# Optimization experiments

Measured on AMD Instinct MI355X. Metric: run time of the kernel, lower is better.

The kernel has to match this reference:

```python
import jax, jax.numpy as jnp
import numpy as np

B, L, R, DV = 4, 4096, 8, 64

def setup_inputs() -> dict:
    key = jax.random.key(0)
    k1, k2, k3, k4 = jax.random.split(key, 4)
    return {
        "v": jax.random.normal(k1, (B, L, DV), dtype=jnp.float32),
        "mask": jax.random.randint(k2, (B, 1, L), 0, 2, dtype=jnp.int32),
        "random_attn_1": jax.random.normal(k3, (B, L, R), dtype=jnp.float32),
        "random_attn_2": jax.random.normal(k4, (B, R, L), dtype=jnp.float32),
        "len_q": L,
    }

def reference(v, mask, random_attn_1, random_attn_2, len_q):
    # rank-8 low-rank synthesis of attention scores: [B, len_q, len_q]
    Bm = mask.shape[0]
    scores = jnp.einsum("blr,brm->blm",
                        random_attn_1[:Bm, :len_q, :],
                        random_attn_2[:Bm, :, :len_q])
    scores = jnp.where(mask == 0, jnp.float32(-1e9), scores)
    attn = jax.nn.softmax(scores, axis=-1)  # dropout omitted (eval mode)
    out = jnp.einsum("blm,bmd->bld", attn, v[:Bm, :len_q, :])
    return out, attn
```

## Files before the change

kernel.cpp:

```cpp
#include <hip/hip_runtime.h>
#include <hip/hip_bf16.h>

#define BB  4
#define LL  4096
#define RR  8
#define DVV 64

typedef __bf16 bf16x8 __attribute__((ext_vector_type(8)));
typedef __bf16 bf16x4 __attribute__((ext_vector_type(4)));
typedef float  f32x4  __attribute__((ext_vector_type(4)));
typedef int    i32x4  __attribute__((ext_vector_type(4)));

#define LGKM_BARRIER() \
  asm volatile("s_waitcnt lgkmcnt(0)\n\ts_barrier" ::: "memory")

__global__ __launch_bounds__(256) void prep_kernel(
    const float* __restrict__ v, __bf16* __restrict__ vF) {
  __shared__ __bf16 tl[64][72];
  const int blk = blockIdx.x;
  const int b   = blk >> 6;
  const int m0  = (blk & 63) << 6;
  const int tid = threadIdx.x;

  const float* vb = v + (((size_t)(b * LL + m0)) << 6);
#pragma unroll
  for (int i = 0; i < 16; ++i) {
    const int idx = (i << 8) + tid;
    tl[idx & 63][idx >> 6] = (__bf16)vb[idx];
  }
  __syncthreads();

  const int wv = tid >> 6, ln = tid & 63;
#pragma unroll
  for (int i = 0; i < 2; ++i) {
    const int u  = wv + (i << 2);
    const int cb = u >> 2, gg = u & 3;
    const int d  = gg * 16 + (ln & 15);
    const int c  = cb * 32 + ((ln >> 4) << 3);
    const size_t unit = ((size_t)(b * 128 + (m0 >> 5) + cb) << 2) + gg;
    *(bf16x8*)(vF + (unit << 9) + (ln << 3)) = *(const bf16x8*)&tl[d][c];
  }
}

__global__ __launch_bounds__(512, 4) void attn_main(
    const float* __restrict__ ra1, const float* __restrict__ ra2,
    const int* __restrict__ mask, const __bf16* __restrict__ vF,
    float* __restrict__ out, float* __restrict__ attn) {
  __shared__ __bf16 pbuf[8 * 8 * 512];
  __shared__ float  red[8][8];

  const int wg   = blockIdx.x;
  const int b    = wg >> 9;
  const int row0 = (wg & 511) << 3;
  const int tid  = threadIdx.x;
  const int wave = tid >> 6;
  const int lane = tid & 63;
  const int W    = wave << 9;

  const float* r2 = ra2 + (size_t)b * (RR * LL) + W + (lane << 2);
  f32x4 rA[RR], rB[RR];
#pragma unroll
  for (int r = 0; r < RR; ++r) {
    rA[r] = *(const f32x4*)(r2 + r * LL);
    rB[r] = *(const f32x4*)(r2 + r * LL + 256);
  }
  const int* mp = mask + (size_t)b * LL + W + (lane << 2);
  const i32x4 mAv = *(const i32x4*)mp;
  const i32x4 mBv = *(const i32x4*)(mp + 256);
  f32x4 mA, mB;
#pragma unroll
  for (int j = 0; j < 4; ++j) {
    mA[j] = mAv[j] ? 1.0f : 0.0f;
    mB[j] = mBv[j] ? 1.0f : 0.0f;
  }

  const float* a_base = ra1 + ((size_t)b * LL + row0) * RR;
  char* const  pw     = (char*)pbuf + (wave << 13);

  float part[8];
#pragma unroll
  for (int i = 0; i < 8; ++i) {
    const float* ap = a_base + i * RR;
    f32x4 sA = {0.f, 0.f, 0.f, 0.f}, sB = {0.f, 0.f, 0.f, 0.f};
#pragma unroll
    for (int r = 0; r < RR; ++r) {
      const float a = ap[r];
#pragma unroll
      for (int j = 0; j < 4; ++j) {
        sA[j] = fmaf(a, rA[r][j], sA[j]);
        sB[j] = fmaf(a, rB[r][j], sB[j]);
      }
    }
    f32x4 eA, eB;
#pragma unroll
    for (int j = 0; j < 4; ++j) {
      eA[j] = __expf(sA[j]) * mA[j];
      eB[j] = __expf(sB[j]) * mB[j];
    }
    part[i] = ((eA[0] + eA[1]) + (eA[2] + eA[3])) +
              ((eB[0] + eB[1]) + (eB[2] + eB[3]));

    bf16x4 pA, pB;
#pragma unroll
    for (int j = 0; j < 4; ++j) { pA[j] = (__bf16)eA[j]; pB[j] = (__bf16)eB[j]; }
    const int swz = (i & 7) << 4;
    *(bf16x4*)(pw + (i << 10) + (((lane << 3)) ^ swz))       = pA;
    *(bf16x4*)(pw + (i << 10) + ((512 + (lane << 3)) ^ swz)) = pB;
  }
#pragma unroll
  for (int s = 1; s < 64; s <<= 1)
#pragma unroll
    for (int i = 0; i < 8; ++i) part[i] += __shfl_xor(part[i], s);
  if (lane == 0) {
#pragma unroll
    for (int i = 0; i < 8; ++i) red[i][wave] = part[i];
  }
  LGKM_BARRIER();

  float rs = 0.f;
#pragma unroll
  for (int v = 0; v < 8; ++v) rs += red[wave][v];
  const float rinv_w = 1.0f / rs;

  const int lrow = lane & 15, kg = lane >> 4;
  const int lr8  = lrow & 7;
  f32x4 acc[4];
#pragma unroll
  for (int g = 0; g < 4; ++g) acc[g] = (f32x4){0.f, 0.f, 0.f, 0.f};
  const __bf16* vFb = vF + ((size_t)b << 18);
  float* arow = attn + ((size_t)b * LL + row0 + wave) * LL;

#pragma unroll
  for (int t = 0; t < 16; ++t) {
    const bf16x8 af = *(const bf16x8*)(
        pw + (lr8 << 10) + (((t << 6) + (kg << 4)) ^ (lr8 << 4)));
    const __bf16* vblk =
        vFb + ((size_t)((wave << 4) + t) << 11) + (lane << 3);
#pragma unroll
    for (int g = 0; g < 4; ++g) {
      const bf16x8 bf = *(const bf16x8*)(vblk + (g << 9));
      acc[g] =
          __builtin_amdgcn_mfma_f32_16x16x32_bf16(af, bf, acc[g], 0, 0, 0);
    }
    const bf16x4 q = *(const bf16x4*)(
        (const char*)pbuf + ((t >> 1) << 13) + (wave << 10) + ((t & 1) << 9) +
        ((lane << 3) ^ ((wave & 7) << 4)));
    f32x4 o;
#pragma unroll
    for (int j = 0; j < 4; ++j) o[j] = (float)q[j] * rinv_w;
    *(f32x4*)(arow + (t << 8) + (lane << 2)) = o;
  }

  LGKM_BARRIER();
  float* osum = (float*)pbuf;
  if (kg < 2) {
#pragma unroll
    for (int g = 0; g < 4; ++g)
#pragma unroll
      for (int ii = 0; ii < 4; ++ii)
        osum[(wave * 8 + kg * 4 + ii) * 64 + g * 16 + lrow] = acc[g][ii];
  }
  LGKM_BARRIER();

  if (tid < 128) {
    const int orow = tid >> 4;
    const int d    = (tid & 15) << 2;
    f32x4 o = {0.f, 0.f, 0.f, 0.f};
#pragma unroll
    for (int w = 0; w < 8; ++w) {
      const f32x4 rr = *(const f32x4*)(osum + ((w * 8 + orow) << 6) + d);
#pragma unroll
      for (int j = 0; j < 4; ++j) o[j] += rr[j];
    }
    float rt = 0.f;
#pragma unroll
    for (int w = 0; w < 8; ++w) rt += red[orow][w];
    const float rinv_o = 1.0f / rt;
#pragma unroll
    for (int j = 0; j < 4; ++j) o[j] *= rinv_o;
    *(f32x4*)(out + ((size_t)b * LL + row0 + orow) * DVV + d) = o;
  }
}

extern "C" void kernel_launch(void* const* d_in, const int* in_sizes, int n_in,
                              void* d_out, int out_size, void* d_ws,
                              size_t ws_size, hipStream_t stream) {
  (void)in_sizes; (void)n_in; (void)out_size; (void)ws_size;
  const float* v    = (const float*)d_in[0];
  const int*   mask = (const int*)d_in[1];
  const float* ra1  = (const float*)d_in[2];
  const float* ra2  = (const float*)d_in[3];

  float* out  = (float*)d_out;
  float* attn = out + (size_t)BB * LL * DVV;

  __bf16* vF = (__bf16*)d_ws;

  hipLaunchKernelGGL(prep_kernel, dim3(BB * (LL / 64)), dim3(256), 0, stream,
                     v, vF);
  hipLaunchKernelGGL(attn_main, dim3(BB * LL / 8), dim3(512), 0, stream,
                     ra1, ra2, mask, vF, out, attn);
}
```

Before: 316.8 us.

## Specialize waves: add store waves for attn output, loop four row blocks per workgroup

The main kernel now launches 512 workgroups of 10 waves, each looping over four 8-row blocks. Eight compute waves do the scores, exp and MFMA while two extra waves handle writing the normalized attention rows. The 8-wave partial output reduction is split into a two-stage reduction through a smaller shared buffer. The intent is to overlap the large attn store traffic with compute and to spread the ra2 register loads across two halves, which lowers register pressure. The cost is more barriers per iteration and fewer workgroups in flight.

```diff
diff --git a/kernel.cpp b/kernel.cpp
--- a/kernel.cpp
+++ b/kernel.cpp
@@ -42,143 +42,183 @@
   }
 }
 
-__global__ __launch_bounds__(512, 4) void attn_main(
+__global__ __launch_bounds__(640, 5) void attn_main(
     const float* __restrict__ ra1, const float* __restrict__ ra2,
     const int* __restrict__ mask, const __bf16* __restrict__ vF,
     float* __restrict__ out, float* __restrict__ attn) {
   __shared__ __bf16 pbuf[8 * 8 * 512];
+  __shared__ float  osum4[4 * 8 * 64];
   __shared__ float  red[8][8];
 
   const int wg   = blockIdx.x;
-  const int b    = wg >> 9;
-  const int row0 = (wg & 511) << 3;
+  const int b    = wg >> 7;
+  const int blk0 = (wg & 127) << 2;
   const int tid  = threadIdx.x;
   const int wave = tid >> 6;
   const int lane = tid & 63;
-  const int W    = wave << 9;
-
-  const float* r2 = ra2 + (size_t)b * (RR * LL) + W + (lane << 2);
-  f32x4 rA[RR], rB[RR];
-#pragma unroll
-  for (int r = 0; r < RR; ++r) {
-    rA[r] = *(const f32x4*)(r2 + r * LL);
-    rB[r] = *(const f32x4*)(r2 + r * LL + 256);
-  }
-  const int* mp = mask + (size_t)b * LL + W + (lane << 2);
-  const i32x4 mAv = *(const i32x4*)mp;
-  const i32x4 mBv = *(const i32x4*)(mp + 256);
-  f32x4 mA, mB;
-#pragma unroll
-  for (int j = 0; j < 4; ++j) {
-    mA[j] = mAv[j] ? 1.0f : 0.0f;
-    mB[j] = mBv[j] ? 1.0f : 0.0f;
-  }
-
-  const float* a_base = ra1 + ((size_t)b * LL + row0) * RR;
-  char* const  pw     = (char*)pbuf + (wave << 13);
-
-  float part[8];
-#pragma unroll
-  for (int i = 0; i < 8; ++i) {
-    const float* ap = a_base + i * RR;
-    f32x4 sA = {0.f, 0.f, 0.f, 0.f}, sB = {0.f, 0.f, 0.f, 0.f};
-#pragma unroll
-    for (int r = 0; r < RR; ++r) {
-      const float a = ap[r];
-#pragma unroll
-      for (int j = 0; j < 4; ++j) {
-        sA[j] = fmaf(a, rA[r][j], sA[j]);
-        sB[j] = fmaf(a, rB[r][j], sB[j]);
-      }
-    }
-    f32x4 eA, eB;
-#pragma unroll
-    for (int j = 0; j < 4; ++j) {
-      eA[j] = __expf(sA[j]) * mA[j];
-      eB[j] = __expf(sB[j]) * mB[j];
-    }
-    part[i] = ((eA[0] + eA[1]) + (eA[2] + eA[3])) +
-              ((eB[0] + eB[1]) + (eB[2] + eB[3]));
-
-    bf16x4 pA, pB;
-#pragma unroll
-    for (int j = 0; j < 4; ++j) { pA[j] = (__bf16)eA[j]; pB[j] = (__bf16)eB[j]; }
-    const int swz = (i & 7) << 4;
-    *(bf16x4*)(pw + (i << 10) + (((lane << 3)) ^ swz))       = pA;
-    *(bf16x4*)(pw + (i << 10) + ((512 + (lane << 3)) ^ swz)) = pB;
-  }
-#pragma unroll
-  for (int s = 1; s < 64; s <<= 1)
-#pragma unroll
-    for (int i = 0; i < 8; ++i) part[i] += __shfl_xor(part[i], s);
-  if (lane == 0) {
-#pragma unroll
-    for (int i = 0; i < 8; ++i) red[i][wave] = part[i];
-  }
-  LGKM_BARRIER();
-
-  float rs = 0.f;
-#pragma unroll
-  for (int v = 0; v < 8; ++v) rs += red[wave][v];
-  const float rinv_w = 1.0f / rs;
-
+  const int cw   = wave & 7;
+  const int W    = cw << 9;
   const int lrow = lane & 15, kg = lane >> 4;
   const int lr8  = lrow & 7;
-  f32x4 acc[4];
-#pragma unroll
-  for (int g = 0; g < 4; ++g) acc[g] = (f32x4){0.f, 0.f, 0.f, 0.f};
+
+  const float* r2 = ra2 + (size_t)b * (RR * LL) + W + (lane << 2);
+  const int*   mp = mask + (size_t)b * LL + W + (lane << 2);
+
+  f32x4 mA = {0.f, 0.f, 0.f, 0.f}, mB = {0.f, 0.f, 0.f, 0.f};
+  if (wave < 8) {
+    const i32x4 mAv = *(const i32x4*)mp;
+    const i32x4 mBv = *(const i32x4*)(mp + 256);
+#pragma unroll
+    for (int j = 0; j < 4; ++j) {
+      mA[j] = mAv[j] ? 1.0f : 0.0f;
+      mB[j] = mBv[j] ? 1.0f : 0.0f;
+    }
+  }
   const __bf16* vFb = vF + ((size_t)b << 18);
-  float* arow = attn + ((size_t)b * LL + row0 + wave) * LL;
-
-#pragma unroll
-  for (int t = 0; t < 16; ++t) {
-    const bf16x8 af = *(const bf16x8*)(
-        pw + (lr8 << 10) + (((t << 6) + (kg << 4)) ^ (lr8 << 4)));
-    const __bf16* vblk =
-        vFb + ((size_t)((wave << 4) + t) << 11) + (lane << 3);
-#pragma unroll
-    for (int g = 0; g < 4; ++g) {
-      const bf16x8 bf = *(const bf16x8*)(vblk + (g << 9));
-      acc[g] =
-          __builtin_amdgcn_mfma_f32_16x16x32_bf16(af, bf, acc[g], 0, 0, 0);
-    }
-    const bf16x4 q = *(const bf16x4*)(
-        (const char*)pbuf + ((t >> 1) << 13) + (wave << 10) + ((t & 1) << 9) +
-        ((lane << 3) ^ ((wave & 7) << 4)));
-    f32x4 o;
-#pragma unroll
-    for (int j = 0; j < 4; ++j) o[j] = (float)q[j] * rinv_w;
-    *(f32x4*)(arow + (t << 8) + (lane << 2)) = o;
-  }
-
-  LGKM_BARRIER();
-  float* osum = (float*)pbuf;
-  if (kg < 2) {
-#pragma unroll
-    for (int g = 0; g < 4; ++g)
-#pragma unroll
-      for (int ii = 0; ii < 4; ++ii)
-        osum[(wave * 8 + kg * 4 + ii) * 64 + g * 16 + lrow] = acc[g][ii];
-  }
-  LGKM_BARRIER();
-
-  if (tid < 128) {
-    const int orow = tid >> 4;
-    const int d    = (tid & 15) << 2;
-    f32x4 o = {0.f, 0.f, 0.f, 0.f};
-#pragma unroll
-    for (int w = 0; w < 8; ++w) {
-      const f32x4 rr = *(const f32x4*)(osum + ((w * 8 + orow) << 6) + d);
-#pragma unroll
-      for (int j = 0; j < 4; ++j) o[j] += rr[j];
-    }
-    float rt = 0.f;
-#pragma unroll
-    for (int w = 0; w < 8; ++w) rt += red[orow][w];
-    const float rinv_o = 1.0f / rt;
-#pragma unroll
-    for (int j = 0; j < 4; ++j) o[j] *= rinv_o;
-    *(f32x4*)(out + ((size_t)b * LL + row0 + orow) * DVV + d) = o;
+  char* const   pw  = (char*)pbuf + (cw << 13);
+
+#pragma unroll 1
+  for (int jj = 0; jj < 4; ++jj) {
+    const int row0 = (blk0 + jj) << 3;
+
+    if (wave < 8) {
+      const float* a_base = ra1 + ((size_t)b * LL + row0) * RR;
+      float part[8];
+      {
+        f32x4 rr_[RR];
+#pragma unroll
+        for (int r = 0; r < RR; ++r) rr_[r] = *(const f32x4*)(r2 + r * LL);
+#pragma unroll
+        for (int i = 0; i < 8; ++i) {
+          const float* ap = a_base + i * RR;
+          f32x4 s = {0.f, 0.f, 0.f, 0.f};
+#pragma unroll
+          for (int r = 0; r < RR; ++r)
+#pragma unroll
+            for (int j = 0; j < 4; ++j) s[j] = fmaf(ap[r], rr_[r][j], s[j]);
+          f32x4 e;
+#pragma unroll
+          for (int j = 0; j < 4; ++j) e[j] = __expf(s[j]) * mA[j];
+          part[i] = (e[0] + e[1]) + (e[2] + e[3]);
+          bf16x4 p;
+#pragma unroll
+          for (int j = 0; j < 4; ++j) p[j] = (__bf16)e[j];
+          *(bf16x4*)(pw + (i << 10) + ((lane << 3) ^ (i << 4))) = p;
+        }
+      }
+      {
+        f32x4 rr_[RR];
+#pragma unroll
+        for (int r = 0; r < RR; ++r)
+          rr_[r] = *(const f32x4*)(r2 + r * LL + 256);
+#pragma unroll
+        for (int i = 0; i < 8; ++i) {
+          const float* ap = a_base + i * RR;
+          f32x4 s = {0.f, 0.f, 0.f, 0.f};
+#pragma unroll
+          for (int r = 0; r < RR; ++r)
+#pragma unroll
+            for (int j = 0; j < 4; ++j) s[j] = fmaf(ap[r], rr_[r][j], s[j]);
+          f32x4 e;
+#pragma unroll
+          for (int j = 0; j < 4; ++j) e[j] = __expf(s[j]) * mB[j];
+          part[i] += (e[0] + e[1]) + (e[2] + e[3]);
+          bf16x4 p;
+#pragma unroll
+          for (int j = 0; j < 4; ++j) p[j] = (__bf16)e[j];
+          *(bf16x4*)(pw + (i << 10) + (512 + ((lane << 3) ^ (i << 4)))) = p;
+        }
+      }
+#pragma unroll
+      for (int s = 1; s < 64; s <<= 1)
+#pragma unroll
+        for (int i = 0; i < 8; ++i) part[i] += __shfl_xor(part[i], s);
+      if (lane == 0) {
+#pragma unroll
+        for (int i = 0; i < 8; ++i) red[i][cw] = part[i];
+      }
+    }
+    LGKM_BARRIER();
+
+    f32x4 acc[4];
+    if (wave < 8) {
+#pragma unroll
+      for (int g = 0; g < 4; ++g) acc[g] = (f32x4){0.f, 0.f, 0.f, 0.f};
+#pragma unroll
+      for (int t = 0; t < 16; ++t) {
+        const bf16x8 af = *(const bf16x8*)(
+            pw + (lr8 << 10) + (((t << 6) + (kg << 4)) ^ (lr8 << 4)));
+        const __bf16* vblk =
+            vFb + ((size_t)((cw << 4) + t) << 11) + (lane << 3);
+#pragma unroll
+        for (int g = 0; g < 4; ++g) {
+          const bf16x8 bf = *(const bf16x8*)(vblk + (g << 9));
+          acc[g] =
+              __builtin_amdgcn_mfma_f32_16x16x32_bf16(af, bf, acc[g], 0, 0, 0);
+        }
+      }
+      if (wave >= 4 && kg < 2) {
+#pragma unroll
+        for (int g = 0; g < 4; ++g)
+#pragma unroll
+          for (int ii = 0; ii < 4; ++ii)
+            osum4[((wave - 4) * 8 + kg * 4 + ii) * 64 + g * 16 + lrow] =
+                acc[g][ii];
+      }
+      LGKM_BARRIER();
+      if (wave < 4 && kg < 2) {
+#pragma unroll
+        for (int g = 0; g < 4; ++g)
+#pragma unroll
+          for (int ii = 0; ii < 4; ++ii)
+            osum4[(wave * 8 + kg * 4 + ii) * 64 + g * 16 + lrow] +=
+                acc[g][ii];
+      }
+    } else {
+      const int w2 = (wave - 8) << 2;
+#pragma unroll
+      for (int rr2 = 0; rr2 < 4; ++rr2) {
+        const int r = w2 + rr2;
+        float rs = 0.f;
+#pragma unroll
+        for (int v2 = 0; v2 < 8; ++v2) rs += red[r][v2];
+        const float rinv_r = 1.0f / rs;
+        float* arow =
+            attn + ((size_t)b * LL + row0 + r) * LL + (lane << 2);
+#pragma unroll
+        for (int t = 0; t < 16; ++t) {
+          const bf16x4 q = *(const bf16x4*)(
+              (const char*)pbuf + ((t >> 1) << 13) + (r << 10) +
+              ((t & 1) << 9) + ((lane << 3) ^ (r << 4)));
+          f32x4 o;
+#pragma unroll
+          for (int j = 0; j < 4; ++j) o[j] = (float)q[j] * rinv_r;
+          *(f32x4*)(arow + (t << 8)) = o;
+        }
+      }
+      LGKM_BARRIER();
+    }
+    LGKM_BARRIER();
+
+    if (tid < 128) {
+      const int orow = tid >> 4;
+      const int d    = (tid & 15) << 2;
+      f32x4 o = {0.f, 0.f, 0.f, 0.f};
+#pragma unroll
+      for (int w = 0; w < 4; ++w) {
+        const f32x4 rr = *(const f32x4*)(osum4 + ((w * 8 + orow) << 6) + d);
+#pragma unroll
+        for (int j = 0; j < 4; ++j) o[j] += rr[j];
+      }
+      float rt = 0.f;
+#pragma unroll
+      for (int w = 0; w < 8; ++w) rt += red[orow][w];
+      const float rinv_o = 1.0f / rt;
+#pragma unroll
+      for (int j = 0; j < 4; ++j) o[j] *= rinv_o;
+      *(f32x4*)(out + ((size_t)b * LL + row0 + orow) * DVV + d) = o;
+    }
+    LGKM_BARRIER();
   }
 }
 
@@ -198,6 +238,6 @@
 
   hipLaunchKernelGGL(prep_kernel, dim3(BB * (LL / 64)), dim3(256), 0, stream,
                      v, vF);
-  hipLaunchKernelGGL(attn_main, dim3(BB * LL / 8), dim3(512), 0, stream,
+  hipLaunchKernelGGL(attn_main, dim3(512), dim3(640), 0, stream,
                      ra1, ra2, mask, vF, out, attn);
 }
```

After: 634.6 us. +100.3%, slower.

## Pipeline attn row stores with score computation in two-row stages

Applied to the files above, without the earlier changes.

Splits the eight-row score computation into four stages of two rows. Each stage gets its own cross-wave sum reduction and barrier, and the normalized attention rows from the previous stage are written out while the next stage computes. Each wave now writes its own column slice of every row instead of whole rows. This spreads the large attn store traffic across the score phase rather than putting it all after the MFMA loop. The cost is four barriers instead of one, plus different store coalescing.

```diff
diff --git a/kernel.cpp b/kernel.cpp
--- a/kernel.cpp
+++ b/kernel.cpp
@@ -76,51 +76,105 @@
 
   const float* a_base = ra1 + ((size_t)b * LL + row0) * RR;
   char* const  pw     = (char*)pbuf + (wave << 13);
-
-  float part[8];
-#pragma unroll
-  for (int i = 0; i < 8; ++i) {
-    const float* ap = a_base + i * RR;
-    f32x4 sA = {0.f, 0.f, 0.f, 0.f}, sB = {0.f, 0.f, 0.f, 0.f};
-#pragma unroll
-    for (int r = 0; r < RR; ++r) {
-      const float a = ap[r];
+  float* attn_base    = attn + ((size_t)b * LL + row0) * LL + W + (lane << 2);
+
+  float rv0 = 0.f, rv1 = 0.f;
+
+#pragma unroll
+  for (int st = 0; st < 4; ++st) {
+    if (st > 0) {
+#pragma unroll
+      for (int h = 0; h < 2; ++h) {
+        const int i   = 2 * (st - 1) + h;
+        const float rv = h ? rv1 : rv0;
+        const int swz = (i & 7) << 4;
+        const bf16x4 qA =
+            *(const bf16x4*)(pw + (i << 10) + ((lane << 3) ^ swz));
+        const bf16x4 qB =
+            *(const bf16x4*)(pw + (i << 10) + (512 + ((lane << 3) ^ swz)));
+        f32x4 oA, oB;
+#pragma unroll
+        for (int j = 0; j < 4; ++j) {
+          oA[j] = (float)qA[j] * rv;
+          oB[j] = (float)qB[j] * rv;
+        }
+        *(f32x4*)(attn_base + (size_t)i * LL)       = oA;
+        *(f32x4*)(attn_base + (size_t)i * LL + 256) = oB;
+      }
+      __builtin_amdgcn_sched_barrier(0);
+    }
+
+    float part[2];
+#pragma unroll
+    for (int h = 0; h < 2; ++h) {
+      const int i = 2 * st + h;
+      const float* ap = a_base + i * RR;
+      f32x4 sA = {0.f, 0.f, 0.f, 0.f}, sB = {0.f, 0.f, 0.f, 0.f};
+#pragma unroll
+      for (int r = 0; r < RR; ++r) {
+        const float a = ap[r];
+#pragma unroll
+        for (int j = 0; j < 4; ++j) {
+          sA[j] = fmaf(a, rA[r][j], sA[j]);
+          sB[j] = fmaf(a, rB[r][j], sB[j]);
+        }
+      }
+      f32x4 eA, eB;
 #pragma unroll
       for (int j = 0; j < 4; ++j) {
-        sA[j] = fmaf(a, rA[r][j], sA[j]);
-        sB[j] = fmaf(a, rB[r][j], sB[j]);
+        eA[j] = __expf(sA[j]) * mA[j];
+        eB[j] = __expf(sB[j]) * mB[j];
       }
-    }
-    f32x4 eA, eB;
+      part[h] = ((eA[0] + eA[1]) + (eA[2] + eA[3])) +
+                ((eB[0] + eB[1]) + (eB[2] + eB[3]));
+
+      bf16x4 pA, pB;
+#pragma unroll
+      for (int j = 0; j < 4; ++j) { pA[j] = (__bf16)eA[j]; pB[j] = (__bf16)eB[j]; }
+      const int swz = (i & 7) << 4;
+      *(bf16x4*)(pw + (i << 10) + ((lane << 3) ^ swz))         = pA;
+      *(bf16x4*)(pw + (i << 10) + (512 + ((lane << 3) ^ swz))) = pB;
+    }
+#pragma unroll
+    for (int s = 1; s < 64; s <<= 1) {
+      part[0] += __shfl_xor(part[0], s);
+      part[1] += __shfl_xor(part[1], s);
+    }
+    if (lane == 0) {
+      red[2 * st][wave]     = part[0];
+      red[2 * st + 1][wave] = part[1];
+    }
+    LGKM_BARRIER();
+    {
+      const f32x4 r00 = *(const f32x4*)&red[2 * st][0];
+      const f32x4 r01 = *(const f32x4*)&red[2 * st][4];
+      const f32x4 r10 = *(const f32x4*)&red[2 * st + 1][0];
+      const f32x4 r11 = *(const f32x4*)&red[2 * st + 1][4];
+      rv0 = 1.0f / (((r00[0] + r00[1]) + (r00[2] + r00[3])) +
+                    ((r01[0] + r01[1]) + (r01[2] + r01[3])));
+      rv1 = 1.0f / (((r10[0] + r10[1]) + (r10[2] + r10[3])) +
+                    ((r11[0] + r11[1]) + (r11[2] + r11[3])));
+    }
+  }
+
+#pragma unroll
+  for (int h = 0; h < 2; ++h) {
+    const int i    = 6 + h;
+    const float rv = h ? rv1 : rv0;
+    const int swz  = (i & 7) << 4;
+    const bf16x4 qA = *(const bf16x4*)(pw + (i << 10) + ((lane << 3) ^ swz));
+    const bf16x4 qB =
+        *(const bf16x4*)(pw + (i << 10) + (512 + ((lane << 3) ^ swz)));
+    f32x4 oA, oB;
 #pragma unroll
     for (int j = 0; j < 4; ++j) {
-      eA[j] = __expf(sA[j]) * mA[j];
-      eB[j] = __expf(sB[j]) * mB[j];
-    }
-    part[i] = ((eA[0] + eA[1]) + (eA[2] + eA[3])) +
-              ((eB[0] + eB[1]) + (eB[2] + eB[3]));
-
-    bf16x4 pA, pB;
-#pragma unroll
-    for (int j = 0; j < 4; ++j) { pA[j] = (__bf16)eA[j]; pB[j] = (__bf16)eB[j]; }
-    const int swz = (i & 7) << 4;
-    *(bf16x4*)(pw + (i << 10) + (((lane << 3)) ^ swz))       = pA;
-    *(bf16x4*)(pw + (i << 10) + ((512 + (lane << 3)) ^ swz)) = pB;
-  }
-#pragma unroll
-  for (int s = 1; s < 64; s <<= 1)
-#pragma unroll
-    for (int i = 0; i < 8; ++i) part[i] += __shfl_xor(part[i], s);
-  if (lane == 0) {
-#pragma unroll
-    for (int i = 0; i < 8; ++i) red[i][wave] = part[i];
-  }
-  LGKM_BARRIER();
-
-  float rs = 0.f;
-#pragma unroll
-  for (int v = 0; v < 8; ++v) rs += red[wave][v];
-  const float rinv_w = 1.0f / rs;
+      oA[j] = (float)qA[j] * rv;
+      oB[j] = (float)qB[j] * rv;
+    }
+    *(f32x4*)(attn_base + (size_t)i * LL)       = oA;
+    *(f32x4*)(attn_base + (size_t)i * LL + 256) = oB;
+  }
+  __builtin_amdgcn_sched_barrier(0);
 
   const int lrow = lane & 15, kg = lane >> 4;
   const int lr8  = lrow & 7;
@@ -128,8 +182,6 @@
 #pragma unroll
   for (int g = 0; g < 4; ++g) acc[g] = (f32x4){0.f, 0.f, 0.f, 0.f};
   const __bf16* vFb = vF + ((size_t)b << 18);
-  float* arow = attn + ((size_t)b * LL + row0 + wave) * LL;
-
 #pragma unroll
   for (int t = 0; t < 16; ++t) {
     const bf16x8 af = *(const bf16x8*)(
@@ -142,13 +194,6 @@
       acc[g] =
           __builtin_amdgcn_mfma_f32_16x16x32_bf16(af, bf, acc[g], 0, 0, 0);
     }
-    const bf16x4 q = *(const bf16x4*)(
-        (const char*)pbuf + ((t >> 1) << 13) + (wave << 10) + ((t & 1) << 9) +
-        ((lane << 3) ^ ((wave & 7) << 4)));
-    f32x4 o;
-#pragma unroll
-    for (int j = 0; j < 4; ++j) o[j] = (float)q[j] * rinv_w;
-    *(f32x4*)(arow + (t << 8) + (lane << 2)) = o;
   }
 
   LGKM_BARRIER();
```

Result: no change. 320.9 us (+1.3%).
